# Optimization experiments

Measured on AMD Instinct MI355X. Metric: run time of the kernel, lower is better.

## Reference

```python
import jax, jax.numpy as jnp
import numpy as np

B, L, D, DK, T = 8192, 64, 512, 64, 128
WIDE_IN = 2 * T + T * T  # 16640


def setup_inputs() -> dict:
    key = jax.random.key(0)
    ks = jax.random.split(key, 24)
    s = 0.02
    inp = {
        "mashup_tags": jax.random.uniform(ks[0], (B, T), jnp.float32),
        "target_api_tags": jax.random.uniform(ks[1], (B, T), jnp.float32),
        "cross_product_tag": jax.random.uniform(ks[2], (B, T * T), jnp.float32),
        "encoded_api_context": jax.random.normal(ks[3], (B, L, D), jnp.float32),
        "candidate_api_description_feature": jax.random.normal(ks[4], (B, D), jnp.float32),
        "mashup_description_feature": jax.random.normal(ks[5], (B, D), jnp.float32),
        "context_len": jax.random.randint(ks[6], (B,), 0, L + 1, jnp.int64 if jax.config.jax_enable_x64 else jnp.int32),
        # attention projections (torch Linear weight layout: [out, in], no bias)
        "W_K": s * jax.random.normal(ks[7], (DK, D), jnp.float32),
        "W_Q": s * jax.random.normal(ks[8], (DK, D), jnp.float32),
        # wide head
        "wide_w": s * jax.random.normal(ks[9], (1, WIDE_IN), jnp.float32),
        "wide_b": jnp.zeros((1,), jnp.float32),
        # deep MLP 1536->512->256->128->1
        "d1_w": s * jax.random.normal(ks[10], (512, 3 * D), jnp.float32),
        "d1_b": jnp.zeros((512,), jnp.float32),
        "d2_w": s * jax.random.normal(ks[11], (256, 512), jnp.float32),
        "d2_b": jnp.zeros((256,), jnp.float32),
        "d3_w": s * jax.random.normal(ks[12], (128, 256), jnp.float32),
        "d3_b": jnp.zeros((128,), jnp.float32),
        "d4_w": s * jax.random.normal(ks[13], (1, 128), jnp.float32),
        "d4_b": jnp.zeros((1,), jnp.float32),
        "wide_weight": jnp.ones((1,), jnp.float32),
        "deep_weight": jnp.ones((1,), jnp.float32),
        "bias": jnp.zeros((1,), jnp.float32),
    }
    return inp


def reference(mashup_tags, target_api_tags, cross_product_tag,
              encoded_api_context, candidate_api_description_feature,
              mashup_description_feature, context_len,
              W_K, W_Q, wide_w, wide_b,
              d1_w, d1_b, d2_w, d2_b, d3_w, d3_b, d4_w, d4_b,
              wide_weight, deep_weight, bias):
    # ---- wide branch ----
    wide_in = jnp.concatenate([mashup_tags, target_api_tags, cross_product_tag], axis=1)
    wide_out = jax.nn.sigmoid(wide_in @ wide_w.T + wide_b)  # (B,1)

    # ---- ragged attention (vectorized masked softmax replaces the Python batch loop) ----
    K = jnp.einsum("bld,kd->blk", encoded_api_context, W_K)          # (B,L,dk)
    Q = candidate_api_description_feature @ W_Q.T                     # (B,dk)
    scores = jnp.einsum("blk,bk->bl", K, Q)                           # (B,L)
    mask = jnp.arange(scores.shape[1])[None, :] < context_len[:, None]
    m = jnp.max(jnp.where(mask, scores, -1e30), axis=-1, keepdims=True)
    e = jnp.where(mask, jnp.exp(scores - m), 0.0)
    denom = jnp.sum(e, axis=-1, keepdims=True)
    probs = e / jnp.maximum(denom, 1e-30)  # rows with length==0 -> all zeros (matches torch zeros fallback)
    api_context = jnp.einsum("bl,bld->bd", probs, encoded_api_context)  # (B,512)

    # ---- deep branch ----
    deep_in = jnp.concatenate([mashup_description_feature, api_context,
                               candidate_api_description_feature], axis=1)  # (B,1536)
    h = jax.nn.relu(deep_in @ d1_w.T + d1_b)
    h = jax.nn.relu(h @ d2_w.T + d2_b)
    h = jax.nn.relu(h @ d3_w.T + d3_b)
    deep_out = h @ d4_w.T + d4_b  # (B,1)

    out = wide_weight * wide_out + deep_weight * deep_out + bias
    return jax.nn.sigmoid(out)
```

## Files before the change

### kernel.cpp

```cpp
#include <hip/hip_runtime.h>

#define Bsz 8192
#define Lctx 64
#define Ddim 512
#define DK 64
#define Ttag 128
#define RQT 4

using f32x4 = __attribute__((ext_vector_type(4))) float;
using bf16x8 = __attribute__((ext_vector_type(8))) short;

__device__ __forceinline__ float wave_sum(float v) {
#pragma unroll
    for (int m = 32; m > 0; m >>= 1) v += __shfl_xor(v, m, 64);
    return v;
}

__device__ __forceinline__ float dot4(float4 a, float4 b) {
    return a.x * b.x + a.y * b.y + a.z * b.z + a.w * b.w;
}

__device__ __forceinline__ unsigned f2bf(float f) {
    unsigned int u = __float_as_uint(f);
    u = u + 0x7fffu + ((u >> 16) & 1u);
    return u >> 16;
}
__device__ __forceinline__ unsigned pack2(float a, float b) {
    return f2bf(a) | (f2bf(b) << 16);
}

__global__ __launch_bounds__(256) void k_prep(
    const float* __restrict__ C, const float* __restrict__ WQ,
    const float* __restrict__ WK, float* __restrict__ qt,
    const float* __restrict__ s1, unsigned short* __restrict__ d1,
    const float* __restrict__ s2, unsigned short* __restrict__ d2,
    const float* __restrict__ s3, unsigned short* __restrict__ d3)
{
    if (blockIdx.x >= 512) {
        int i = (blockIdx.x - 512) * 256 + threadIdx.x;
        const float* s;
        unsigned short* d;
        if (i < 196608)      { s = s1; d = d1; }
        else if (i < 229376) { i -= 196608; s = s2; d = d2; }
        else                 { i -= 229376; s = s3; d = d3; }
        const float4 v = ((const float4*)s)[i];
        uint2 w;
        w.x = pack2(v.x, v.y);
        w.y = pack2(v.z, v.w);
        *(uint2*)&d[(size_t)i * 4] = w;
        return;
    }

    const int lane = threadIdx.x & 63;
    const int gw = blockIdx.x * 4 + (threadIdx.x >> 6);
    const int b0 = gw * RQT;

    float4 c0[RQT], c1[RQT];
#pragma unroll
    for (int r = 0; r < RQT; ++r) {
        const float4* row = (const float4*)(C + (size_t)(b0 + r) * Ddim);
        c0[r] = row[lane];
        c1[r] = row[64 + lane];
    }
    float tv[RQT];
#pragma unroll
    for (int r = 0; r < RQT; ++r) tv[r] = 0.f;
    for (int k = 0; k < DK; ++k) {
        const float4* wrow = (const float4*)(WQ + (size_t)k * Ddim);
        const float4 w0 = wrow[lane];
        const float4 w1 = wrow[64 + lane];
#pragma unroll
        for (int r = 0; r < RQT; ++r) {
            float p = dot4(c0[r], w0) + dot4(c1[r], w1);
            p = wave_sum(p);
            if (lane == k) tv[r] = p;
        }
    }
    float4 a0[RQT], a1[RQT];
#pragma unroll
    for (int r = 0; r < RQT; ++r) {
        a0[r] = make_float4(0.f, 0.f, 0.f, 0.f);
        a1[r] = make_float4(0.f, 0.f, 0.f, 0.f);
    }
    for (int k = 0; k < DK; ++k) {
        const float4* wrow = (const float4*)(WK + (size_t)k * Ddim);
        const float4 w0 = wrow[lane];
        const float4 w1 = wrow[64 + lane];
#pragma unroll
        for (int r = 0; r < RQT; ++r) {
            const float tk = __shfl(tv[r], k, 64);
            a0[r].x += tk * w0.x; a0[r].y += tk * w0.y;
            a0[r].z += tk * w0.z; a0[r].w += tk * w0.w;
            a1[r].x += tk * w1.x; a1[r].y += tk * w1.y;
            a1[r].z += tk * w1.z; a1[r].w += tk * w1.w;
        }
    }
#pragma unroll
    for (int r = 0; r < RQT; ++r) {
        float4* orow = (float4*)(qt + (size_t)(b0 + r) * Ddim);
        orow[lane] = a0[r];
        orow[64 + lane] = a1[r];
    }
}

__global__ __launch_bounds__(256) void k_attn_wide(
    const float* __restrict__ X, const float* __restrict__ qt,
    const int* __restrict__ clen, const float* __restrict__ mdesc,
    const float* __restrict__ cand,
    const float* __restrict__ mt, const float* __restrict__ tt,
    const float* __restrict__ cp, const float* __restrict__ ww,
    const float* __restrict__ wb,
    unsigned short* __restrict__ din, float* __restrict__ wl)
{
    const int tid = threadIdx.x;
    const int wave = tid >> 6, lane = tid & 63;
    const int b = blockIdx.x * 4 + wave;
    const int len = clen[b];

    const float4* qrow = (const float4*)(qt + (size_t)b * Ddim);
    const float4 q0 = qrow[lane];
    const float4 q1 = qrow[64 + lane];
    const float4* xb = (const float4*)(X + (size_t)b * Lctx * Ddim);
    const float4* cp4 = (const float4*)(cp + (size_t)b * (Ttag * Ttag));
    const float4* ww4 = (const float4*)(ww + 2 * Ttag);

    float wacc;
    {
        const float2 a  = ((const float2*)(mt + (size_t)b * Ttag))[lane];
        const float2 wA = ((const float2*)ww)[lane];
        const float2 t  = ((const float2*)(tt + (size_t)b * Ttag))[lane];
        const float2 wB = ((const float2*)(ww + Ttag))[lane];
        wacc = a.x * wA.x + a.y * wA.y + t.x * wB.x + t.y * wB.y;
    }

    float4 y0 = make_float4(0.f, 0.f, 0.f, 0.f);
    float4 y1 = make_float4(0.f, 0.f, 0.f, 0.f);
    float M = -1e30f, D = 0.f;

    for (int c = 0; c < 16; ++c) {
        const int base = c * 4;
        const int nr = min(4, len - base);

        float4 t0[4], t1[4];
        if (nr > 0) {
#pragma unroll
            for (int r = 0; r < 4; ++r) {
                const int l = base + min(r, nr - 1);
                t0[r] = xb[l * 128 + lane];
                t1[r] = xb[l * 128 + 64 + lane];
            }
        }
        float4 cv[4], wv[4];
#pragma unroll
        for (int i = 0; i < 4; ++i) {
            cv[i] = cp4[(c * 4 + i) * 64 + lane];
            wv[i] = ww4[(c * 4 + i) * 64 + lane];
        }

        if (nr > 0) {
            float sc[4];
#pragma unroll
            for (int r = 0; r < 4; ++r)
                sc[r] = dot4(t0[r], q0) + dot4(t1[r], q1);
#pragma unroll
            for (int r = 0; r < 4; ++r) sc[r] = wave_sum(sc[r]);

            float pmax = -1e30f;
#pragma unroll
            for (int r = 0; r < 4; ++r)
                if (r < nr) pmax = fmaxf(pmax, sc[r]);
            const float Mn = fmaxf(M, pmax);
            const float scale = __expf(M - Mn);
            D *= scale;
            y0.x *= scale; y0.y *= scale; y0.z *= scale; y0.w *= scale;
            y1.x *= scale; y1.y *= scale; y1.z *= scale; y1.w *= scale;
#pragma unroll
            for (int r = 0; r < 4; ++r) {
                if (r < nr) {
                    const float e = __expf(sc[r] - Mn);
                    D += e;
                    y0.x += e * t0[r].x; y0.y += e * t0[r].y;
                    y0.z += e * t0[r].z; y0.w += e * t0[r].w;
                    y1.x += e * t1[r].x; y1.y += e * t1[r].y;
                    y1.z += e * t1[r].z; y1.w += e * t1[r].w;
                }
            }
            M = Mn;
        }
#pragma unroll
        for (int i = 0; i < 4; ++i) wacc += dot4(cv[i], wv[i]);
    }

    wacc = wave_sum(wacc);
    if (lane == 0) wl[b] = wacc + wb[0];

    unsigned short* dr = din + (size_t)b * 1536;
    const float rden = 1.f / fmaxf(D, 1e-30f);
    {
        uint2 w;
        w.x = pack2(y0.x * rden, y0.y * rden);
        w.y = pack2(y0.z * rden, y0.w * rden);
        *(uint2*)&dr[512 + 4 * lane] = w;
        w.x = pack2(y1.x * rden, y1.y * rden);
        w.y = pack2(y1.z * rden, y1.w * rden);
        *(uint2*)&dr[512 + 256 + 4 * lane] = w;
    }
    {
        const float4* md = (const float4*)(mdesc + (size_t)b * Ddim);
        const float4 m0 = md[lane], m1 = md[64 + lane];
        uint2 w;
        w.x = pack2(m0.x, m0.y); w.y = pack2(m0.z, m0.w);
        *(uint2*)&dr[4 * lane] = w;
        w.x = pack2(m1.x, m1.y); w.y = pack2(m1.z, m1.w);
        *(uint2*)&dr[256 + 4 * lane] = w;
    }
    {
        const float4* cd = (const float4*)(cand + (size_t)b * Ddim);
        const float4 c0 = cd[lane], c1 = cd[64 + lane];
        uint2 w;
        w.x = pack2(c0.x, c0.y); w.y = pack2(c0.z, c0.w);
        *(uint2*)&dr[1024 + 4 * lane] = w;
        w.x = pack2(c1.x, c1.y); w.y = pack2(c1.z, c1.w);
        *(uint2*)&dr[1024 + 256 + 4 * lane] = w;
    }
}

template <int BN>
__global__ __launch_bounds__(256) void k_gemm_bf16(
    const unsigned short* __restrict__ A, const unsigned short* __restrict__ W,
    const float* __restrict__ bias, unsigned short* __restrict__ C,
    const int K, const int N, const int relu)
{
    constexpr int WN = BN / 2;
    constexpr int NN = WN / 16;
    constexpr int NB = (BN * 8) / 256;
    __shared__ unsigned short As[128][72];
    __shared__ unsigned short Bs[BN][72];
    const int tid = threadIdx.x;
    const int wave = tid >> 6, lane = tid & 63;
    const int wm = wave >> 1, wn = wave & 1;
    const size_t m0 = (size_t)blockIdx.x * 128;
    const size_t n0 = (size_t)blockIdx.y * BN;

    f32x4 acc[4][NN];
#pragma unroll
    for (int i = 0; i < 4; ++i)
#pragma unroll
        for (int j = 0; j < NN; ++j) acc[i][j] = (f32x4){0.f, 0.f, 0.f, 0.f};

    uint4 pa[4], pb[NB];
    auto loadA = [&](int k0) {
#pragma unroll
        for (int j = 0; j < 4; ++j) {
            const int i = tid + j * 256;
            const int row = i >> 3, c8 = (i & 7) * 8;
            pa[j] = *(const uint4*)(A + (m0 + row) * (size_t)K + k0 + c8);
        }
    };
    auto loadB = [&](int k0) {
#pragma unroll
        for (int j = 0; j < NB; ++j) {
            const int i = tid + j * 256;
            const int row = i >> 3, c8 = (i & 7) * 8;
            pb[j] = *(const uint4*)(W + (n0 + row) * (size_t)K + k0 + c8);
        }
    };

    loadA(0);
    loadB(0);
    for (int k0 = 0; k0 < K; k0 += 64) {
        __syncthreads();
#pragma unroll
        for (int j = 0; j < 4; ++j) {
            const int i = tid + j * 256;
            const int row = i >> 3, c8 = (i & 7) * 8;
            *(uint4*)&As[row][c8] = pa[j];
        }
#pragma unroll
        for (int j = 0; j < NB; ++j) {
            const int i = tid + j * 256;
            const int row = i >> 3, c8 = (i & 7) * 8;
            *(uint4*)&Bs[row][c8] = pb[j];
        }
        __syncthreads();
        if (k0 + 64 < K) { loadA(k0 + 64); loadB(k0 + 64); }
#pragma unroll
        for (int kk = 0; kk < 2; ++kk) {
            const int krow = kk * 32 + (lane >> 4) * 8;
            bf16x8 af[4], bfr[NN];
#pragma unroll
            for (int mm = 0; mm < 4; ++mm)
                af[mm] = *(const bf16x8*)&As[wm * 64 + mm * 16 + (lane & 15)][krow];
#pragma unroll
            for (int nn = 0; nn < NN; ++nn)
                bfr[nn] = *(const bf16x8*)&Bs[wn * WN + nn * 16 + (lane & 15)][krow];
#pragma unroll
            for (int mm = 0; mm < 4; ++mm)
#pragma unroll
                for (int nn = 0; nn < NN; ++nn)
                    acc[mm][nn] = __builtin_amdgcn_mfma_f32_16x16x32_bf16(
                        af[mm], bfr[nn], acc[mm][nn], 0, 0, 0);
        }
    }

#pragma unroll
    for (int nn = 0; nn < NN; ++nn) {
        const int col = (int)n0 + wn * WN + nn * 16 + (lane & 15);
        const float bv = bias[col];
#pragma unroll
        for (int mm = 0; mm < 4; ++mm) {
#pragma unroll
            for (int r = 0; r < 4; ++r) {
                const size_t row = m0 + wm * 64 + mm * 16 + (lane >> 4) * 4 + r;
                float v = acc[mm][nn][r] + bv;
                if (relu) v = fmaxf(v, 0.f);
                C[row * N + col] = (unsigned short)f2bf(v);
            }
        }
    }
}

__global__ __launch_bounds__(256) void k_gemm3_final(
    const unsigned short* __restrict__ A, const unsigned short* __restrict__ W,
    const float* __restrict__ bias, const float* __restrict__ d4w,
    const float* __restrict__ d4b, const float* __restrict__ wl,
    const float* __restrict__ wwt, const float* __restrict__ dwt,
    const float* __restrict__ bs, float* __restrict__ out)
{
    constexpr int K = 256, N = 128;
    __shared__ unsigned short As[128][72];
    __shared__ unsigned short Bs[128][72];
    __shared__ float dp[128][2];
    const int tid = threadIdx.x;
    const int wave = tid >> 6, lane = tid & 63;
    const int wm = wave >> 1, wn = wave & 1;
    const size_t m0 = (size_t)blockIdx.x * 128;

    f32x4 acc[4][4];
#pragma unroll
    for (int i = 0; i < 4; ++i)
#pragma unroll
        for (int j = 0; j < 4; ++j) acc[i][j] = (f32x4){0.f, 0.f, 0.f, 0.f};

    uint4 pa[4], pb[4];
    auto loadA = [&](int k0) {
#pragma unroll
        for (int j = 0; j < 4; ++j) {
            const int i = tid + j * 256;
            const int row = i >> 3, c8 = (i & 7) * 8;
            pa[j] = *(const uint4*)(A + (m0 + row) * (size_t)K + k0 + c8);
        }
    };
    auto loadB = [&](int k0) {
#pragma unroll
        for (int j = 0; j < 4; ++j) {
            const int i = tid + j * 256;
            const int row = i >> 3, c8 = (i & 7) * 8;
            pb[j] = *(const uint4*)(W + row * (size_t)K + k0 + c8);
        }
    };

    loadA(0);
    loadB(0);
    for (int k0 = 0; k0 < K; k0 += 64) {
        __syncthreads();
#pragma unroll
        for (int j = 0; j < 4; ++j) {
            const int i = tid + j * 256;
            const int row = i >> 3, c8 = (i & 7) * 8;
            *(uint4*)&As[row][c8] = pa[j];
            *(uint4*)&Bs[row][c8] = pb[j];
        }
        __syncthreads();
        if (k0 + 64 < K) { loadA(k0 + 64); loadB(k0 + 64); }
#pragma unroll
        for (int kk = 0; kk < 2; ++kk) {
            const int krow = kk * 32 + (lane >> 4) * 8;
            bf16x8 af[4], bfr[4];
#pragma unroll
            for (int mm = 0; mm < 4; ++mm)
                af[mm] = *(const bf16x8*)&As[wm * 64 + mm * 16 + (lane & 15)][krow];
#pragma unroll
            for (int nn = 0; nn < 4; ++nn)
                bfr[nn] = *(const bf16x8*)&Bs[wn * 64 + nn * 16 + (lane & 15)][krow];
#pragma unroll
            for (int mm = 0; mm < 4; ++mm)
#pragma unroll
                for (int nn = 0; nn < 4; ++nn)
                    acc[mm][nn] = __builtin_amdgcn_mfma_f32_16x16x32_bf16(
                        af[mm], bfr[nn], acc[mm][nn], 0, 0, 0);
        }
    }

    float rowpart[4][4];
#pragma unroll
    for (int mm = 0; mm < 4; ++mm)
#pragma unroll
        for (int r = 0; r < 4; ++r) rowpart[mm][r] = 0.f;
#pragma unroll
    for (int nn = 0; nn < 4; ++nn) {
        const int col = wn * 64 + nn * 16 + (lane & 15);
        const float bv = bias[col];
        const float w4 = d4w[col];
#pragma unroll
        for (int mm = 0; mm < 4; ++mm)
#pragma unroll
            for (int r = 0; r < 4; ++r) {
                float v = acc[mm][nn][r] + bv;
                v = fmaxf(v, 0.f);
                rowpart[mm][r] += v * w4;
            }
    }
#pragma unroll
    for (int mm = 0; mm < 4; ++mm)
#pragma unroll
        for (int r = 0; r < 4; ++r) {
            float v = rowpart[mm][r];
            v += __shfl_xor(v, 1, 64);
            v += __shfl_xor(v, 2, 64);
            v += __shfl_xor(v, 4, 64);
            v += __shfl_xor(v, 8, 64);
            if ((lane & 15) == 0)
                dp[wm * 64 + mm * 16 + (lane >> 4) * 4 + r][wn] = v;
        }
    __syncthreads();
    if (tid < 128) {
        const int row = tid;
        const float deep = dp[row][0] + dp[row][1] + d4b[0];
        const size_t b = m0 + row;
        const float wo = 1.f / (1.f + __expf(-wl[b]));
        const float z = wwt[0] * wo + dwt[0] * deep + bs[0];
        out[b] = 1.f / (1.f + __expf(-z));
    }
}

extern "C" void kernel_launch(void* const* d_in, const int* in_sizes, int n_in,
                              void* d_out, int out_size, void* d_ws, size_t ws_size,
                              hipStream_t stream)
{
    const float* mt    = (const float*)d_in[0];
    const float* tt    = (const float*)d_in[1];
    const float* cp    = (const float*)d_in[2];
    const float* X     = (const float*)d_in[3];
    const float* cand  = (const float*)d_in[4];
    const float* mdesc = (const float*)d_in[5];
    const int*   clen  = (const int*)d_in[6];
    const float* WK    = (const float*)d_in[7];
    const float* WQ    = (const float*)d_in[8];
    const float* ww    = (const float*)d_in[9];
    const float* wb    = (const float*)d_in[10];
    const float* d1w   = (const float*)d_in[11];
    const float* d1b   = (const float*)d_in[12];
    const float* d2w   = (const float*)d_in[13];
    const float* d2b   = (const float*)d_in[14];
    const float* d3w   = (const float*)d_in[15];
    const float* d3b   = (const float*)d_in[16];
    const float* d4w   = (const float*)d_in[17];
    const float* d4b   = (const float*)d_in[18];
    const float* wwt   = (const float*)d_in[19];
    const float* dwt   = (const float*)d_in[20];
    const float* bs    = (const float*)d_in[21];
    float* out = (float*)d_out;

    char* w = (char*)d_ws;
    unsigned short* din = (unsigned short*)w;            w += (size_t)Bsz * 1536 * 2;
    float* qt           = (float*)w;                     w += (size_t)Bsz * 512 * 4;
    unsigned short* h1  = (unsigned short*)w;            w += (size_t)Bsz * 512 * 2;
    unsigned short* h2  = (unsigned short*)w;            w += (size_t)Bsz * 256 * 2;
    float* wl           = (float*)w;                     w += (size_t)Bsz * 4;
    unsigned short* w1b = (unsigned short*)w;            w += (size_t)512 * 1536 * 2;
    unsigned short* w2b = (unsigned short*)w;            w += (size_t)256 * 512 * 2;
    unsigned short* w3b = (unsigned short*)w;            w += (size_t)128 * 256 * 2;

    hipLaunchKernelGGL(k_prep, dim3(1440), dim3(256), 0, stream,
                       cand, WQ, WK, qt, d1w, w1b, d2w, w2b, d3w, w3b);
    hipLaunchKernelGGL(k_attn_wide, dim3(Bsz / 4), dim3(256), 0, stream,
                       X, qt, clen, mdesc, cand, mt, tt, cp, ww, wb, din, wl);
    hipLaunchKernelGGL((k_gemm_bf16<64>), dim3(64, 8), dim3(256), 0, stream,
                       din, w1b, d1b, h1, 1536, 512, 1);
    hipLaunchKernelGGL((k_gemm_bf16<64>), dim3(64, 4), dim3(256), 0, stream,
                       h1, w2b, d2b, h2, 512, 256, 1);
    hipLaunchKernelGGL(k_gemm3_final, dim3(64), dim3(256), 0, stream,
                       h2, w3b, d3b, d4w, d4b, wl, wwt, dwt, bs, out);
}
```

Before: 451.6 us.

## Split each attention row across eight waves with two-pass softmax via shared memory

The attention/wide kernel now assigns one batch row per 512-thread block instead of one row per wave. Each wave handles a strided subset of context rows, computes their scores, and keeps the rows in registers as packed bf16. One wave then does the exact softmax from shared memory, and the weighted sums are reduced across waves through shared memory. The wide cross-product dot is also spread over all 512 threads. This removes the serial online-softmax chain and the per-wave sequential streaming, so more loads can be in flight. In exchange it adds block barriers and shared-memory traffic, and rounds the context rows to bf16 before the weighted sum.

After: 435.9 us. 1.04x faster.

```diff
diff --git a/kernel.cpp b/kernel.cpp
--- a/kernel.cpp
+++ b/kernel.cpp
@@ -28,6 +28,8 @@
 __device__ __forceinline__ unsigned pack2(float a, float b) {
     return f2bf(a) | (f2bf(b) << 16);
 }
+__device__ __forceinline__ float bflo(unsigned int v) { return __uint_as_float(v << 16); }
+__device__ __forceinline__ float bfhi(unsigned int v) { return __uint_as_float(v & 0xffff0000u); }
 
 __global__ __launch_bounds__(256) void k_prep(
     const float* __restrict__ C, const float* __restrict__ WQ,
@@ -103,7 +105,7 @@
     }
 }
 
-__global__ __launch_bounds__(256) void k_attn_wide(
+__global__ __launch_bounds__(512, 2) void k_attn_wide(
     const float* __restrict__ X, const float* __restrict__ qt,
     const int* __restrict__ clen, const float* __restrict__ mdesc,
     const float* __restrict__ cand,
@@ -112,117 +114,122 @@
     const float* __restrict__ wb,
     unsigned short* __restrict__ din, float* __restrict__ wl)
 {
+    __shared__ float sl[Lctx];
+    __shared__ float pl[Lctx];
+    __shared__ float part[8][Ddim];
+    __shared__ float red[8];
+
+    const int b = blockIdx.x;
     const int tid = threadIdx.x;
     const int wave = tid >> 6, lane = tid & 63;
-    const int b = blockIdx.x * 4 + wave;
     const int len = clen[b];
+    const int nrw = (len > wave) ? ((len - wave + 7) >> 3) : 0;
 
     const float4* qrow = (const float4*)(qt + (size_t)b * Ddim);
     const float4 q0 = qrow[lane];
     const float4 q1 = qrow[64 + lane];
     const float4* xb = (const float4*)(X + (size_t)b * Lctx * Ddim);
-    const float4* cp4 = (const float4*)(cp + (size_t)b * (Ttag * Ttag));
-    const float4* ww4 = (const float4*)(ww + 2 * Ttag);
-
-    float wacc;
+
+    uint2 pk[8][2];
+    float sc[8];
+
+    if (nrw > 0) {
+        float4 t0[8], t1[8];
+#pragma unroll
+        for (int k = 0; k < 8; ++k) {
+            if (k < nrw) {
+                const int l = wave + k * 8;
+                t0[k] = xb[l * 128 + lane];
+                t1[k] = xb[l * 128 + 64 + lane];
+            }
+        }
+#pragma unroll
+        for (int k = 0; k < 8; ++k) {
+            if (k < nrw) {
+                sc[k] = dot4(t0[k], q0) + dot4(t1[k], q1);
+                pk[k][0].x = pack2(t0[k].x, t0[k].y);
+                pk[k][0].y = pack2(t0[k].z, t0[k].w);
+                pk[k][1].x = pack2(t1[k].x, t1[k].y);
+                pk[k][1].y = pack2(t1[k].z, t1[k].w);
+            }
+        }
+#pragma unroll
+        for (int k = 0; k < 8; ++k)
+            if (k < nrw) sc[k] = wave_sum(sc[k]);
+        if (lane == 0) {
+#pragma unroll
+            for (int k = 0; k < 8; ++k)
+                if (k < nrw) sl[wave + k * 8] = sc[k];
+        }
+    }
+
+    float wacc = 0.f;
+    if (tid < 64) {
+        float4 v;
+        if (tid < 32) v = ((const float4*)(mt + (size_t)b * Ttag))[tid];
+        else          v = ((const float4*)(tt + (size_t)b * Ttag))[tid - 32];
+        wacc += dot4(v, ((const float4*)ww)[tid]);
+    }
     {
-        const float2 a  = ((const float2*)(mt + (size_t)b * Ttag))[lane];
-        const float2 wA = ((const float2*)ww)[lane];
-        const float2 t  = ((const float2*)(tt + (size_t)b * Ttag))[lane];
-        const float2 wB = ((const float2*)(ww + Ttag))[lane];
-        wacc = a.x * wA.x + a.y * wA.y + t.x * wB.x + t.y * wB.y;
-    }
-
-    float4 y0 = make_float4(0.f, 0.f, 0.f, 0.f);
-    float4 y1 = make_float4(0.f, 0.f, 0.f, 0.f);
-    float M = -1e30f, D = 0.f;
-
-    for (int c = 0; c < 16; ++c) {
-        const int base = c * 4;
-        const int nr = min(4, len - base);
-
-        float4 t0[4], t1[4];
-        if (nr > 0) {
-#pragma unroll
-            for (int r = 0; r < 4; ++r) {
-                const int l = base + min(r, nr - 1);
-                t0[r] = xb[l * 128 + lane];
-                t1[r] = xb[l * 128 + 64 + lane];
-            }
-        }
-        float4 cv[4], wv[4];
-#pragma unroll
-        for (int i = 0; i < 4; ++i) {
-            cv[i] = cp4[(c * 4 + i) * 64 + lane];
-            wv[i] = ww4[(c * 4 + i) * 64 + lane];
-        }
-
-        if (nr > 0) {
-            float sc[4];
-#pragma unroll
-            for (int r = 0; r < 4; ++r)
-                sc[r] = dot4(t0[r], q0) + dot4(t1[r], q1);
-#pragma unroll
-            for (int r = 0; r < 4; ++r) sc[r] = wave_sum(sc[r]);
-
-            float pmax = -1e30f;
-#pragma unroll
-            for (int r = 0; r < 4; ++r)
-                if (r < nr) pmax = fmaxf(pmax, sc[r]);
-            const float Mn = fmaxf(M, pmax);
-            const float scale = __expf(M - Mn);
-            D *= scale;
-            y0.x *= scale; y0.y *= scale; y0.z *= scale; y0.w *= scale;
-            y1.x *= scale; y1.y *= scale; y1.z *= scale; y1.w *= scale;
-#pragma unroll
-            for (int r = 0; r < 4; ++r) {
-                if (r < nr) {
-                    const float e = __expf(sc[r] - Mn);
-                    D += e;
-                    y0.x += e * t0[r].x; y0.y += e * t0[r].y;
-                    y0.z += e * t0[r].z; y0.w += e * t0[r].w;
-                    y1.x += e * t1[r].x; y1.y += e * t1[r].y;
-                    y1.z += e * t1[r].z; y1.w += e * t1[r].w;
-                }
-            }
-            M = Mn;
-        }
-#pragma unroll
-        for (int i = 0; i < 4; ++i) wacc += dot4(cv[i], wv[i]);
-    }
-
+        const float4* cp4 = (const float4*)(cp + (size_t)b * (Ttag * Ttag));
+        const float4* ww4 = (const float4*)(ww + 2 * Ttag);
+#pragma unroll 4
+        for (int i = tid; i < (Ttag * Ttag) / 4; i += 512)
+            wacc += dot4(cp4[i], ww4[i]);
+    }
     wacc = wave_sum(wacc);
-    if (lane == 0) wl[b] = wacc + wb[0];
+    if (lane == 0) red[wave] = wacc;
+
+    __syncthreads();
+
+    if (wave == 0) {
+        const float s = (lane < len) ? sl[lane] : -1e30f;
+        float m = s;
+#pragma unroll
+        for (int msk = 32; msk > 0; msk >>= 1)
+            m = fmaxf(m, __shfl_xor(m, msk, 64));
+        const float e = (lane < len) ? __expf(s - m) : 0.f;
+        const float d = wave_sum(e);
+        pl[lane] = e * (1.f / fmaxf(d, 1e-30f));
+    }
+    __syncthreads();
+
+    float4 a0 = make_float4(0.f, 0.f, 0.f, 0.f);
+    float4 a1 = make_float4(0.f, 0.f, 0.f, 0.f);
+#pragma unroll
+    for (int k = 0; k < 8; ++k) {
+        if (k < nrw) {
+            const float p = pl[wave + k * 8];
+            a0.x += p * bflo(pk[k][0].x); a0.y += p * bfhi(pk[k][0].x);
+            a0.z += p * bflo(pk[k][0].y); a0.w += p * bfhi(pk[k][0].y);
+            a1.x += p * bflo(pk[k][1].x); a1.y += p * bfhi(pk[k][1].x);
+            a1.z += p * bflo(pk[k][1].y); a1.w += p * bfhi(pk[k][1].y);
+        }
+    }
+    *(float4*)&part[wave][lane * 4] = a0;
+    *(float4*)&part[wave][256 + lane * 4] = a1;
+    __syncthreads();
 
     unsigned short* dr = din + (size_t)b * 1536;
-    const float rden = 1.f / fmaxf(D, 1e-30f);
     {
+        float v = 0.f;
+#pragma unroll
+        for (int w8 = 0; w8 < 8; ++w8) v += part[w8][tid];
+        dr[512 + tid] = (unsigned short)f2bf(v);
+    }
+    if (tid < 256) {
+        const float4 v = (tid < 128)
+            ? ((const float4*)(mdesc + (size_t)b * Ddim))[tid]
+            : ((const float4*)(cand + (size_t)b * Ddim))[tid - 128];
         uint2 w;
-        w.x = pack2(y0.x * rden, y0.y * rden);
-        w.y = pack2(y0.z * rden, y0.w * rden);
-        *(uint2*)&dr[512 + 4 * lane] = w;
-        w.x = pack2(y1.x * rden, y1.y * rden);
-        w.y = pack2(y1.z * rden, y1.w * rden);
-        *(uint2*)&dr[512 + 256 + 4 * lane] = w;
-    }
-    {
-        const float4* md = (const float4*)(mdesc + (size_t)b * Ddim);
-        const float4 m0 = md[lane], m1 = md[64 + lane];
-        uint2 w;
-        w.x = pack2(m0.x, m0.y); w.y = pack2(m0.z, m0.w);
-        *(uint2*)&dr[4 * lane] = w;
-        w.x = pack2(m1.x, m1.y); w.y = pack2(m1.z, m1.w);
-        *(uint2*)&dr[256 + 4 * lane] = w;
-    }
-    {
-        const float4* cd = (const float4*)(cand + (size_t)b * Ddim);
-        const float4 c0 = cd[lane], c1 = cd[64 + lane];
-        uint2 w;
-        w.x = pack2(c0.x, c0.y); w.y = pack2(c0.z, c0.w);
-        *(uint2*)&dr[1024 + 4 * lane] = w;
-        w.x = pack2(c1.x, c1.y); w.y = pack2(c1.z, c1.w);
-        *(uint2*)&dr[1024 + 256 + 4 * lane] = w;
-    }
+        w.x = pack2(v.x, v.y);
+        w.y = pack2(v.z, v.w);
+        const int off = (tid < 128) ? tid * 4 : 1024 + (tid - 128) * 4;
+        *(uint2*)&dr[off] = w;
+    }
+    if (tid == 0)
+        wl[b] = red[0] + red[1] + red[2] + red[3] +
+                red[4] + red[5] + red[6] + red[7] + wb[0];
 }
 
 template <int BN>
@@ -474,7 +481,7 @@
 
     hipLaunchKernelGGL(k_prep, dim3(1440), dim3(256), 0, stream,
                        cand, WQ, WK, qt, d1w, w1b, d2w, w2b, d3w, w3b);
-    hipLaunchKernelGGL(k_attn_wide, dim3(Bsz / 4), dim3(256), 0, stream,
+    hipLaunchKernelGGL(k_attn_wide, dim3(Bsz), dim3(512), 0, stream,
                        X, qt, clen, mdesc, cand, mt, tt, cp, ww, wb, din, wl);
     hipLaunchKernelGGL((k_gemm_bf16<64>), dim3(64, 8), dim3(256), 0, stream,
                        din, w1b, d1b, h1, 1536, 512, 1);
```

## Split fused attention/wide kernel into score, wide, and weighted-sum kernels

Applied to the files above, without the earlier changes.

Replaces the single online-softmax kernel that also computed the wide dot product with three kernels. One computes attention scores into a workspace, one does the wide cross-product reduction with a block per batch row, and one does a full softmax and weighted sum. The aim is more parallelism and simpler per-kernel work instead of serialized online-softmax rescaling. In exchange, the context tensor is read twice and extra launches and a scores buffer are added.

Result: slower. 547.3 us (+21.2%).

```diff
diff --git a/kernel.cpp b/kernel.cpp
--- a/kernel.cpp
+++ b/kernel.cpp
@@ -13,6 +13,12 @@
 __device__ __forceinline__ float wave_sum(float v) {
 #pragma unroll
     for (int m = 32; m > 0; m >>= 1) v += __shfl_xor(v, m, 64);
+    return v;
+}
+
+__device__ __forceinline__ float wave_max(float v) {
+#pragma unroll
+    for (int m = 32; m > 0; m >>= 1) v = fmaxf(v, __shfl_xor(v, m, 64));
     return v;
 }
 
@@ -103,14 +109,9 @@
     }
 }
 
-__global__ __launch_bounds__(256) void k_attn_wide(
+__global__ __launch_bounds__(256, 6) void k_score(
     const float* __restrict__ X, const float* __restrict__ qt,
-    const int* __restrict__ clen, const float* __restrict__ mdesc,
-    const float* __restrict__ cand,
-    const float* __restrict__ mt, const float* __restrict__ tt,
-    const float* __restrict__ cp, const float* __restrict__ ww,
-    const float* __restrict__ wb,
-    unsigned short* __restrict__ din, float* __restrict__ wl)
+    const int* __restrict__ clen, float* __restrict__ scores)
 {
     const int tid = threadIdx.x;
     const int wave = tid >> 6, lane = tid & 63;
@@ -121,88 +122,80 @@
     const float4 q0 = qrow[lane];
     const float4 q1 = qrow[64 + lane];
     const float4* xb = (const float4*)(X + (size_t)b * Lctx * Ddim);
-    const float4* cp4 = (const float4*)(cp + (size_t)b * (Ttag * Ttag));
-    const float4* ww4 = (const float4*)(ww + 2 * Ttag);
-
-    float wacc;
-    {
-        const float2 a  = ((const float2*)(mt + (size_t)b * Ttag))[lane];
-        const float2 wA = ((const float2*)ww)[lane];
-        const float2 t  = ((const float2*)(tt + (size_t)b * Ttag))[lane];
-        const float2 wB = ((const float2*)(ww + Ttag))[lane];
-        wacc = a.x * wA.x + a.y * wA.y + t.x * wB.x + t.y * wB.y;
-    }
-
+
+    for (int base = 0; base < len; base += 4) {
+        const int rem = len - base;
+        float4 t0[4], t1[4];
+#pragma unroll
+        for (int r = 0; r < 4; ++r) {
+            const int l = base + min(r, rem - 1);
+            t0[r] = xb[l * 128 + lane];
+            t1[r] = xb[l * 128 + 64 + lane];
+        }
+        float sc[4];
+#pragma unroll
+        for (int r = 0; r < 4; ++r)
+            sc[r] = dot4(t0[r], q0) + dot4(t1[r], q1);
+#pragma unroll
+        for (int r = 0; r < 4; ++r) sc[r] = wave_sum(sc[r]);
+        if (lane == 0) {
+#pragma unroll
+            for (int r = 0; r < 4; ++r)
+                if (r < rem) scores[(size_t)b * Lctx + base + r] = sc[r];
+        }
+    }
+}
+
+__global__ __launch_bounds__(256, 6) void k_wsum(
+    const float* __restrict__ X, const float* __restrict__ scores,
+    const int* __restrict__ clen, const float* __restrict__ mdesc,
+    const float* __restrict__ cand, unsigned short* __restrict__ din)
+{
+    const int tid = threadIdx.x;
+    const int wave = tid >> 6, lane = tid & 63;
+    const int b = blockIdx.x * 4 + wave;
+    const int len = clen[b];
+
+    const float sraw = scores[(size_t)b * Lctx + lane];
+    const float s = (lane < len) ? sraw : -1e30f;
+    const float m = wave_max(s);
+    const float e = (lane < len) ? __expf(s - m) : 0.f;
+    const float D = wave_sum(e);
+    const float p = e * (1.f / fmaxf(D, 1e-30f));
+
+    const float4* xb = (const float4*)(X + (size_t)b * Lctx * Ddim);
     float4 y0 = make_float4(0.f, 0.f, 0.f, 0.f);
     float4 y1 = make_float4(0.f, 0.f, 0.f, 0.f);
-    float M = -1e30f, D = 0.f;
-
-    for (int c = 0; c < 16; ++c) {
-        const int base = c * 4;
-        const int nr = min(4, len - base);
-
+
+    for (int base = 0; base < len; base += 4) {
+        const int rem = len - base;
         float4 t0[4], t1[4];
-        if (nr > 0) {
-#pragma unroll
-            for (int r = 0; r < 4; ++r) {
-                const int l = base + min(r, nr - 1);
-                t0[r] = xb[l * 128 + lane];
-                t1[r] = xb[l * 128 + 64 + lane];
+#pragma unroll
+        for (int r = 0; r < 4; ++r) {
+            const int l = base + min(r, rem - 1);
+            t0[r] = xb[l * 128 + lane];
+            t1[r] = xb[l * 128 + 64 + lane];
+        }
+#pragma unroll
+        for (int r = 0; r < 4; ++r) {
+            if (r < rem) {
+                const float pl = __shfl(p, base + r, 64);
+                y0.x += pl * t0[r].x; y0.y += pl * t0[r].y;
+                y0.z += pl * t0[r].z; y0.w += pl * t0[r].w;
+                y1.x += pl * t1[r].x; y1.y += pl * t1[r].y;
+                y1.z += pl * t1[r].z; y1.w += pl * t1[r].w;
             }
         }
-        float4 cv[4], wv[4];
-#pragma unroll
-        for (int i = 0; i < 4; ++i) {
-            cv[i] = cp4[(c * 4 + i) * 64 + lane];
-            wv[i] = ww4[(c * 4 + i) * 64 + lane];
-        }
-
-        if (nr > 0) {
-            float sc[4];
-#pragma unroll
-            for (int r = 0; r < 4; ++r)
-                sc[r] = dot4(t0[r], q0) + dot4(t1[r], q1);
-#pragma unroll
-            for (int r = 0; r < 4; ++r) sc[r] = wave_sum(sc[r]);
-
-            float pmax = -1e30f;
-#pragma unroll
-            for (int r = 0; r < 4; ++r)
-                if (r < nr) pmax = fmaxf(pmax, sc[r]);
-            const float Mn = fmaxf(M, pmax);
-            const float scale = __expf(M - Mn);
-            D *= scale;
-            y0.x *= scale; y0.y *= scale; y0.z *= scale; y0.w *= scale;
-            y1.x *= scale; y1.y *= scale; y1.z *= scale; y1.w *= scale;
-#pragma unroll
-            for (int r = 0; r < 4; ++r) {
-                if (r < nr) {
-                    const float e = __expf(sc[r] - Mn);
-                    D += e;
-                    y0.x += e * t0[r].x; y0.y += e * t0[r].y;
-                    y0.z += e * t0[r].z; y0.w += e * t0[r].w;
-                    y1.x += e * t1[r].x; y1.y += e * t1[r].y;
-                    y1.z += e * t1[r].z; y1.w += e * t1[r].w;
-                }
-            }
-            M = Mn;
-        }
-#pragma unroll
-        for (int i = 0; i < 4; ++i) wacc += dot4(cv[i], wv[i]);
-    }
-
-    wacc = wave_sum(wacc);
-    if (lane == 0) wl[b] = wacc + wb[0];
+    }
 
     unsigned short* dr = din + (size_t)b * 1536;
-    const float rden = 1.f / fmaxf(D, 1e-30f);
     {
         uint2 w;
-        w.x = pack2(y0.x * rden, y0.y * rden);
-        w.y = pack2(y0.z * rden, y0.w * rden);
+        w.x = pack2(y0.x, y0.y);
+        w.y = pack2(y0.z, y0.w);
         *(uint2*)&dr[512 + 4 * lane] = w;
-        w.x = pack2(y1.x * rden, y1.y * rden);
-        w.y = pack2(y1.z * rden, y1.w * rden);
+        w.x = pack2(y1.x, y1.y);
+        w.y = pack2(y1.z, y1.w);
         *(uint2*)&dr[512 + 256 + 4 * lane] = w;
     }
     {
@@ -223,6 +216,33 @@
         w.x = pack2(c1.x, c1.y); w.y = pack2(c1.z, c1.w);
         *(uint2*)&dr[1024 + 256 + 4 * lane] = w;
     }
+}
+
+__global__ __launch_bounds__(256) void k_wide(
+    const float* __restrict__ mt, const float* __restrict__ tt,
+    const float* __restrict__ cp, const float* __restrict__ ww,
+    const float* __restrict__ wb, float* __restrict__ wl)
+{
+    const int b = blockIdx.x;
+    const int tid = threadIdx.x;
+    const int wave = tid >> 6, lane = tid & 63;
+    float acc = 0.f;
+    if (tid < 64) {
+        float4 v;
+        if (tid < 32) v = ((const float4*)(mt + (size_t)b * Ttag))[tid];
+        else          v = ((const float4*)(tt + (size_t)b * Ttag))[tid - 32];
+        acc += dot4(v, ((const float4*)ww)[tid]);
+    }
+    const float4* cp4 = (const float4*)(cp + (size_t)b * (Ttag * Ttag));
+    const float4* ww4 = (const float4*)(ww + 2 * Ttag);
+#pragma unroll 4
+    for (int i = tid; i < (Ttag * Ttag) / 4; i += 256)
+        acc += dot4(cp4[i], ww4[i]);
+    acc = wave_sum(acc);
+    __shared__ float red[4];
+    if (lane == 0) red[wave] = acc;
+    __syncthreads();
+    if (tid == 0) wl[b] = red[0] + red[1] + red[2] + red[3] + wb[0];
 }
 
 template <int BN>
@@ -468,14 +488,19 @@
     unsigned short* h1  = (unsigned short*)w;            w += (size_t)Bsz * 512 * 2;
     unsigned short* h2  = (unsigned short*)w;            w += (size_t)Bsz * 256 * 2;
     float* wl           = (float*)w;                     w += (size_t)Bsz * 4;
+    float* scores       = (float*)w;                     w += (size_t)Bsz * Lctx * 4;
     unsigned short* w1b = (unsigned short*)w;            w += (size_t)512 * 1536 * 2;
     unsigned short* w2b = (unsigned short*)w;            w += (size_t)256 * 512 * 2;
     unsigned short* w3b = (unsigned short*)w;            w += (size_t)128 * 256 * 2;
 
     hipLaunchKernelGGL(k_prep, dim3(1440), dim3(256), 0, stream,
                        cand, WQ, WK, qt, d1w, w1b, d2w, w2b, d3w, w3b);
-    hipLaunchKernelGGL(k_attn_wide, dim3(Bsz / 4), dim3(256), 0, stream,
-                       X, qt, clen, mdesc, cand, mt, tt, cp, ww, wb, din, wl);
+    hipLaunchKernelGGL(k_score, dim3(Bsz / 4), dim3(256), 0, stream,
+                       X, qt, clen, scores);
+    hipLaunchKernelGGL(k_wide, dim3(Bsz), dim3(256), 0, stream,
+                       mt, tt, cp, ww, wb, wl);
+    hipLaunchKernelGGL(k_wsum, dim3(Bsz / 4), dim3(256), 0, stream,
+                       X, scores, clen, mdesc, cand, din);
     hipLaunchKernelGGL((k_gemm_bf16<64>), dim3(64, 8), dim3(256), 0, stream,
                        din, w1b, d1b, h1, 1536, 512, 1);
     hipLaunchKernelGGL((k_gemm_bf16<64>), dim3(64, 4), dim3(256), 0, stream,
```
